# Kernel optimization log

Measured on AMD Instinct MI355X. Metric: run time of the kernel, lower is better.

## Reference

```python
import jax, jax.numpy as jnp
import numpy as np


def _make_coord(n):
    # pixel-center coords in [-1, 1] (LIIF-style make_coord)
    r = 1.0 / n
    return -1.0 + r + 2.0 * r * jnp.arange(n, dtype=jnp.float32)


def _grid_sample_bilinear(g, xs, ys):
    # g: (Cg, Gh, Gw); xs: (W,) x-coords in [-1,1]; ys: (H,) y-coords.
    # align_corners=True mapping: [-1,1] -> [0, size-1]
    Cg, Gh, Gw = g.shape
    ix = (xs + 1.0) * 0.5 * (Gw - 1)
    iy = (ys + 1.0) * 0.5 * (Gh - 1)
    ix0 = jnp.clip(jnp.floor(ix).astype(jnp.int32), 0, Gw - 1)
    iy0 = jnp.clip(jnp.floor(iy).astype(jnp.int32), 0, Gh - 1)
    ix1 = jnp.clip(ix0 + 1, 0, Gw - 1)
    iy1 = jnp.clip(iy0 + 1, 0, Gh - 1)
    wx = ix - ix0.astype(jnp.float32)  # (W,)
    wy = iy - iy0.astype(jnp.float32)  # (H,)
    # gather 4 corners -> (Cg, H, W)
    g00 = g[:, iy0[:, None], ix0[None, :]]
    g01 = g[:, iy0[:, None], ix1[None, :]]
    g10 = g[:, iy1[:, None], ix0[None, :]]
    g11 = g[:, iy1[:, None], ix1[None, :]]
    wx = wx[None, None, :]
    wy = wy[None, :, None]
    return (g00 * (1 - wy) * (1 - wx) + g01 * (1 - wy) * wx
            + g10 * wy * (1 - wx) + g11 * wy * wx)


def setup_inputs() -> dict:
    key = jax.random.key(0)
    ks = jax.random.split(key, 12)
    B, C, H, W = 8, 32, 256, 256
    hidden, out_dim = 64, 3
    tot_in = C + 16 * 4
    inp = {
        "feat": jax.random.normal(ks[0], (B, C, H, W), dtype=jnp.float32),
        "g0": jax.random.normal(ks[1], (16, 32, 32), dtype=jnp.float32) * 0.1,
        "g1": jax.random.normal(ks[2], (16, 64, 64), dtype=jnp.float32) * 0.1,
        "g2": jax.random.normal(ks[3], (16, 128, 128), dtype=jnp.float32) * 0.1,
        "g3": jax.random.normal(ks[4], (16, 256, 256), dtype=jnp.float32) * 0.1,
        "w1": jax.random.normal(ks[5], (hidden, tot_in), dtype=jnp.float32) * (1.0 / np.sqrt(tot_in)),
        "b1": jnp.zeros((hidden,), dtype=jnp.float32),
        "w2": jax.random.normal(ks[6], (hidden, hidden), dtype=jnp.float32) * (1.0 / np.sqrt(hidden)),
        "b2": jnp.zeros((hidden,), dtype=jnp.float32),
        "w3": jax.random.normal(ks[7], (out_dim, hidden), dtype=jnp.float32) * (1.0 / np.sqrt(hidden)),
        "b3": jnp.zeros((out_dim,), dtype=jnp.float32),
    }
    return inp


def reference(feat, g0, g1, g2, g3, w1, b1, w2, b2, w3, b3):
    B, C, H, W = feat.shape
    xs = _make_coord(W)
    ys = _make_coord(H)
    # grids are shared across batch (expand in torch) -> compute once
    local = jnp.concatenate(
        [_grid_sample_bilinear(g, xs, ys) for g in (g0, g1, g2, g3)], axis=0)  # (64,H,W)
    combined = jnp.concatenate(
        [feat, jnp.broadcast_to(local[None], (B,) + local.shape)], axis=1)  # (B,C+64,H,W)
    x = combined.transpose(0, 2, 3, 1)  # (B,H,W,C+64)
    h = jax.nn.relu(x @ w1.T + b1)
    h = jax.nn.relu(h @ w2.T + b2)
    out = h @ w3.T + b3
    return out.transpose(0, 3, 1, 2)  # (B,out_dim,H,W)
```

## Files before the change

### kernel.cpp

```cpp
#include <hip/hip_runtime.h>
#include <hip/hip_bf16.h>


typedef float f32x4 __attribute__((ext_vector_type(4)));
typedef short s16x8 __attribute__((ext_vector_type(8)));

#define MFMA16(a, b, c) __builtin_amdgcn_mfma_f32_16x16x32_bf16((a), (b), (c), 0, 0, 0)

__device__ __forceinline__ short bfbits(float f) {
    return __builtin_bit_cast(short, __float2bfloat16(f));
}

__device__ __forceinline__ s16x8 pack_relu(const f32x4 lo, const f32x4 hi) {
    s16x8 r;
#pragma unroll
    for (int e = 0; e < 4; ++e) {
        r[e]     = bfbits(fmaxf(lo[e], 0.0f));
        r[e + 4] = bfbits(fmaxf(hi[e], 0.0f));
    }
    return r;
}

#define NFRAG 22

__global__ __launch_bounds__(256, 4) void grid_inr_mfma(
    const float* __restrict__ feat,
    const float* __restrict__ g0, const float* __restrict__ g1,
    const float* __restrict__ g2, const float* __restrict__ g3,
    const float* __restrict__ w1, const float* __restrict__ b1,
    const float* __restrict__ w2, const float* __restrict__ b2,
    const float* __restrict__ w3, const float* __restrict__ b3,
    float* __restrict__ out)
{
    __shared__ __align__(16) short lds_w[NFRAG * 64 * 8];

    const int lane  = threadIdx.x & 63;
    const int col   = lane & 15;
    const int lrow  = lane >> 4;
    const int wv    = threadIdx.x >> 6;
    const int p     = blockIdx.x * 64 + wv * 16 + col;

    {
        const int cs = lane, c15 = lane & 15, r4 = lane >> 4;
#pragma unroll 1
        for (int fid = threadIdx.x >> 6; fid < NFRAG; fid += 4) {
            const float* src;
            if (fid < 12) {
                const int mt = fid / 3, kb = fid - 3 * mt;
                src = w1 + (16 * mt + c15) * 96 + 32 * kb + 4 * r4;
            } else if (fid < 20) {
                const int f = fid - 12, mt = f >> 1, kb = f & 1;
                src = w2 + (16 * mt + c15) * 64 + 32 * kb + 4 * r4;
            } else {
                const int kb = fid - 20;
                const int row3 = (c15 < 3) ? c15 : 2;
                src = w3 + row3 * 64 + 32 * kb + 4 * r4;
            }
            s16x8 frag;
#pragma unroll
            for (int e = 0; e < 8; ++e)
                frag[e] = bfbits(src[(e & 3) + 16 * (e >> 2)]);
            *(s16x8*)&lds_w[(fid * 64 + cs) * 8] = frag;
        }
    }

    f32x4 b1f[4], b2f[4];
#pragma unroll
    for (int mt = 0; mt < 4; ++mt) {
        b1f[mt] = *(const f32x4*)(b1 + 16 * mt + 4 * lrow);
        b2f[mt] = *(const f32x4*)(b2 + 16 * mt + 4 * lrow);
    }
    const float b3s0 = b3[0], b3s1 = b3[1], b3s2 = b3[2];

    s16x8 localB[2];
    {
        const float* gs[4] = {g0, g1, g2, g3};
        const int    gn[4] = {32, 64, 128, 256};
        const int px = p & 255;
        const int py = p >> 8;
#pragma unroll
        for (int lv = 0; lv < 4; ++lv) {
            const int G = gn[lv];
            const float ix = (float)((2 * px + 1) * (G - 1)) * (1.0f / 512.0f);
            const float iy = (float)((2 * py + 1) * (G - 1)) * (1.0f / 512.0f);
            int ix0 = (int)ix;
            int iy0 = (int)iy;
            if (ix0 > G - 1) ix0 = G - 1;
            if (iy0 > G - 1) iy0 = G - 1;
            const int ix1 = (ix0 + 1 < G - 1) ? (ix0 + 1) : (G - 1);
            const int iy1 = (iy0 + 1 < G - 1) ? (iy0 + 1) : (G - 1);
            const float wx = ix - (float)ix0;
            const float wy = iy - (float)iy0;
            const float w00 = (1.0f - wy) * (1.0f - wx);
            const float w01 = (1.0f - wy) * wx;
            const float w10 = wy * (1.0f - wx);
            const float w11 = wy * wx;
            const int o00 = iy0 * G + ix0;
            const int o01 = iy0 * G + ix1;
            const int o10 = iy1 * G + ix0;
            const int o11 = iy1 * G + ix1;
            const float* g = gs[lv];
            const int GG = G * G;
#pragma unroll
            for (int j = 0; j < 4; ++j) {
                const float* gc = g + (4 * lrow + j) * GG;
                const float v = gc[o00] * w00 + gc[o01] * w01 +
                                gc[o10] * w10 + gc[o11] * w11;
                localB[lv >> 1][(lv & 1) * 4 + j] = bfbits(v);
            }
        }
    }

    __syncthreads();

    const short* lw = lds_w + lane * 8;
#define LDSFRAG(fid) (*(const s16x8*)(lw + (fid) * 64 * 8))

    s16x8 w1ff[4], w3f[2];
#pragma unroll
    for (int mt = 0; mt < 4; ++mt) w1ff[mt] = LDSFRAG(mt * 3);
    w3f[0] = LDSFRAG(20);
    w3f[1] = LDSFRAG(21);

    f32x4 c1base[4];
#pragma unroll
    for (int mt = 0; mt < 4; ++mt) {
        c1base[mt] = b1f[mt];
        c1base[mt] = MFMA16(LDSFRAG(mt * 3 + 1), localB[0], c1base[mt]);
        c1base[mt] = MFMA16(LDSFRAG(mt * 3 + 2), localB[1], c1base[mt]);
    }

    auto process = [&](int b, const s16x8 ff) {
        f32x4 c1[4];
#pragma unroll
        for (int mt = 0; mt < 4; ++mt)
            c1[mt] = MFMA16(w1ff[mt], ff, c1base[mt]);

        s16x8 h1b0 = pack_relu(c1[0], c1[1]);
        s16x8 h1b1 = pack_relu(c1[2], c1[3]);

        f32x4 c2[4];
#pragma unroll
        for (int mt = 0; mt < 4; ++mt) {
            c2[mt] = b2f[mt];
            c2[mt] = MFMA16(LDSFRAG(12 + mt * 2),     h1b0, c2[mt]);
            c2[mt] = MFMA16(LDSFRAG(12 + mt * 2 + 1), h1b1, c2[mt]);
        }
        s16x8 h2b0 = pack_relu(c2[0], c2[1]);
        s16x8 h2b1 = pack_relu(c2[2], c2[3]);

        f32x4 c3 = {0.f, 0.f, 0.f, 0.f};
        c3 = MFMA16(w3f[0], h2b0, c3);
        c3 = MFMA16(w3f[1], h2b1, c3);

        if (lrow == 0) {
            out[((b * 3 + 0) << 16) + p] = c3[0] + b3s0;
            out[((b * 3 + 1) << 16) + p] = c3[1] + b3s1;
            out[((b * 3 + 2) << 16) + p] = c3[2] + b3s2;
        }
    };

    float rawP[8], rawQ[8];
#pragma unroll
    for (int e = 0; e < 8; ++e) {
        const int fc = 4 * lrow + (e & 3) + 16 * (e >> 2);
        rawP[e] = feat[(fc << 16) + p];
        rawQ[e] = feat[((32 + fc) << 16) + p];
    }

#pragma unroll 1
    for (int bp = 0; bp < 4; ++bp) {
        s16x8 ff;
#pragma unroll
        for (int e = 0; e < 8; ++e) ff[e] = bfbits(rawP[e]);
        if (bp < 3) {
#pragma unroll
            for (int e = 0; e < 8; ++e) {
                const int fc = 4 * lrow + (e & 3) + 16 * (e >> 2);
                rawP[e] = feat[((((2 * bp + 2) << 5) | fc) << 16) + p];
            }
        }
        process(2 * bp, ff);

#pragma unroll
        for (int e = 0; e < 8; ++e) ff[e] = bfbits(rawQ[e]);
        if (bp < 3) {
#pragma unroll
            for (int e = 0; e < 8; ++e) {
                const int fc = 4 * lrow + (e & 3) + 16 * (e >> 2);
                rawQ[e] = feat[((((2 * bp + 3) << 5) | fc) << 16) + p];
            }
        }
        process(2 * bp + 1, ff);
    }
#undef LDSFRAG
}

extern "C" void kernel_launch(void* const* d_in, const int* in_sizes, int n_in,
                              void* d_out, int out_size, void* d_ws, size_t ws_size,
                              hipStream_t stream) {
    const float* feat = (const float*)d_in[0];
    const float* g0   = (const float*)d_in[1];
    const float* g1   = (const float*)d_in[2];
    const float* g2   = (const float*)d_in[3];
    const float* g3   = (const float*)d_in[4];
    const float* w1   = (const float*)d_in[5];
    const float* b1   = (const float*)d_in[6];
    const float* w2   = (const float*)d_in[7];
    const float* b2   = (const float*)d_in[8];
    const float* w3   = (const float*)d_in[9];
    const float* b3   = (const float*)d_in[10];

    grid_inr_mfma<<<1024, 256, 0, stream>>>(
        feat, g0, g1, g2, g3, w1, b1, w2, b2, w3, b3, (float*)d_out);
}
```

Before: 28.75 us.

## Software-pipeline MLP layer-1 across batches and move b2 and weight frags to LDS

Restructures the batch loop so the layer-1 MFMAs for the next batch run while the current batch's layer-2/3 tail runs, interleaving independent MFMA chains. The b2 bias moves to LDS and the w1ff/w3 fragments are re-read from LDS instead of living in registers, which cuts register pressure at the cost of extra LDS reads. The initial feature loads are issued before the barrier so global latency overlaps the weight staging.

```diff
diff --git a/kernel.cpp b/kernel.cpp
--- a/kernel.cpp
+++ b/kernel.cpp
@@ -33,6 +33,7 @@
     float* __restrict__ out)
 {
     __shared__ __align__(16) short lds_w[NFRAG * 64 * 8];
+    __shared__ __align__(16) float lds_b2[64];
 
     const int lane  = threadIdx.x & 63;
     const int col   = lane & 15;
@@ -40,6 +41,7 @@
     const int wv    = threadIdx.x >> 6;
     const int p     = blockIdx.x * 64 + wv * 16 + col;
 
+    if (threadIdx.x < 64) lds_b2[threadIdx.x] = b2[threadIdx.x];
     {
         const int cs = lane, c15 = lane & 15, r4 = lane >> 4;
 #pragma unroll 1
@@ -64,12 +66,6 @@
         }
     }
 
-    f32x4 b1f[4], b2f[4];
-#pragma unroll
-    for (int mt = 0; mt < 4; ++mt) {
-        b1f[mt] = *(const f32x4*)(b1 + 16 * mt + 4 * lrow);
-        b2f[mt] = *(const f32x4*)(b2 + 16 * mt + 4 * lrow);
-    }
     const float b3s0 = b3[0], b3s1 = b3[1], b3s2 = b3[2];
 
     s16x8 localB[2];
@@ -111,48 +107,40 @@
         }
     }
 
+    float rawP[8], rawQ[8];
+#pragma unroll
+    for (int e = 0; e < 8; ++e) {
+        const int fc = 4 * lrow + (e & 3) + 16 * (e >> 2);
+        rawP[e] = feat[(fc << 16) + p];
+        rawQ[e] = feat[((32 + fc) << 16) + p];
+    }
+
     __syncthreads();
 
     const short* lw = lds_w + lane * 8;
 #define LDSFRAG(fid) (*(const s16x8*)(lw + (fid) * 64 * 8))
 
-    s16x8 w1ff[4], w3f[2];
-#pragma unroll
-    for (int mt = 0; mt < 4; ++mt) w1ff[mt] = LDSFRAG(mt * 3);
-    w3f[0] = LDSFRAG(20);
-    w3f[1] = LDSFRAG(21);
-
     f32x4 c1base[4];
 #pragma unroll
     for (int mt = 0; mt < 4; ++mt) {
-        c1base[mt] = b1f[mt];
+        c1base[mt] = *(const f32x4*)(b1 + 16 * mt + 4 * lrow);
         c1base[mt] = MFMA16(LDSFRAG(mt * 3 + 1), localB[0], c1base[mt]);
         c1base[mt] = MFMA16(LDSFRAG(mt * 3 + 2), localB[1], c1base[mt]);
     }
 
-    auto process = [&](int b, const s16x8 ff) {
-        f32x4 c1[4];
-#pragma unroll
-        for (int mt = 0; mt < 4; ++mt)
-            c1[mt] = MFMA16(w1ff[mt], ff, c1base[mt]);
-
-        s16x8 h1b0 = pack_relu(c1[0], c1[1]);
-        s16x8 h1b1 = pack_relu(c1[2], c1[3]);
-
+    auto tail = [&](int b, const s16x8 h0, const s16x8 h1) {
         f32x4 c2[4];
 #pragma unroll
         for (int mt = 0; mt < 4; ++mt) {
-            c2[mt] = b2f[mt];
-            c2[mt] = MFMA16(LDSFRAG(12 + mt * 2),     h1b0, c2[mt]);
-            c2[mt] = MFMA16(LDSFRAG(12 + mt * 2 + 1), h1b1, c2[mt]);
-        }
-        s16x8 h2b0 = pack_relu(c2[0], c2[1]);
-        s16x8 h2b1 = pack_relu(c2[2], c2[3]);
-
+            const f32x4 bb = *(const f32x4*)&lds_b2[16 * mt + 4 * lrow];
+            c2[mt] = MFMA16(LDSFRAG(12 + 2 * mt + 1), h1,
+                            MFMA16(LDSFRAG(12 + 2 * mt), h0, bb));
+        }
+        const s16x8 h2b0 = pack_relu(c2[0], c2[1]);
+        const s16x8 h2b1 = pack_relu(c2[2], c2[3]);
         f32x4 c3 = {0.f, 0.f, 0.f, 0.f};
-        c3 = MFMA16(w3f[0], h2b0, c3);
-        c3 = MFMA16(w3f[1], h2b1, c3);
-
+        c3 = MFMA16(LDSFRAG(20), h2b0, c3);
+        c3 = MFMA16(LDSFRAG(21), h2b1, c3);
         if (lrow == 0) {
             out[((b * 3 + 0) << 16) + p] = c3[0] + b3s0;
             out[((b * 3 + 1) << 16) + p] = c3[1] + b3s1;
@@ -160,38 +148,61 @@
         }
     };
 
-    float rawP[8], rawQ[8];
-#pragma unroll
-    for (int e = 0; e < 8; ++e) {
-        const int fc = 4 * lrow + (e & 3) + 16 * (e >> 2);
-        rawP[e] = feat[(fc << 16) + p];
-        rawQ[e] = feat[((32 + fc) << 16) + p];
+    f32x4 c1A[4], c1B[4];
+    {
+        s16x8 ffA;
+#pragma unroll
+        for (int e = 0; e < 8; ++e) ffA[e] = bfbits(rawP[e]);
+#pragma unroll
+        for (int e = 0; e < 8; ++e) {
+            const int fc = 4 * lrow + (e & 3) + 16 * (e >> 2);
+            rawP[e] = feat[(((2 << 5) | fc) << 16) + p];
+        }
+#pragma unroll
+        for (int mt = 0; mt < 4; ++mt)
+            c1A[mt] = MFMA16(LDSFRAG(mt * 3), ffA, c1base[mt]);
     }
 
 #pragma unroll 1
     for (int bp = 0; bp < 4; ++bp) {
-        s16x8 ff;
-#pragma unroll
-        for (int e = 0; e < 8; ++e) ff[e] = bfbits(rawP[e]);
-        if (bp < 3) {
-#pragma unroll
-            for (int e = 0; e < 8; ++e) {
-                const int fc = 4 * lrow + (e & 3) + 16 * (e >> 2);
-                rawP[e] = feat[((((2 * bp + 2) << 5) | fc) << 16) + p];
-            }
-        }
-        process(2 * bp, ff);
-
-#pragma unroll
-        for (int e = 0; e < 8; ++e) ff[e] = bfbits(rawQ[e]);
-        if (bp < 3) {
-#pragma unroll
-            for (int e = 0; e < 8; ++e) {
-                const int fc = 4 * lrow + (e & 3) + 16 * (e >> 2);
-                rawQ[e] = feat[((((2 * bp + 3) << 5) | fc) << 16) + p];
-            }
-        }
-        process(2 * bp + 1, ff);
+        {
+            const s16x8 h1A0 = pack_relu(c1A[0], c1A[1]);
+            const s16x8 h1A1 = pack_relu(c1A[2], c1A[3]);
+            s16x8 ffB;
+#pragma unroll
+            for (int e = 0; e < 8; ++e) ffB[e] = bfbits(rawQ[e]);
+            if (bp < 3) {
+#pragma unroll
+                for (int e = 0; e < 8; ++e) {
+                    const int fc = 4 * lrow + (e & 3) + 16 * (e >> 2);
+                    rawQ[e] = feat[((((2 * bp + 3) << 5) | fc) << 16) + p];
+                }
+            }
+#pragma unroll
+            for (int mt = 0; mt < 4; ++mt)
+                c1B[mt] = MFMA16(LDSFRAG(mt * 3), ffB, c1base[mt]);
+            tail(2 * bp, h1A0, h1A1);
+        }
+        {
+            const s16x8 h1B0 = pack_relu(c1B[0], c1B[1]);
+            const s16x8 h1B1 = pack_relu(c1B[2], c1B[3]);
+            if (bp < 3) {
+                s16x8 ffA;
+#pragma unroll
+                for (int e = 0; e < 8; ++e) ffA[e] = bfbits(rawP[e]);
+                if (bp < 2) {
+#pragma unroll
+                    for (int e = 0; e < 8; ++e) {
+                        const int fc = 4 * lrow + (e & 3) + 16 * (e >> 2);
+                        rawP[e] = feat[((((2 * bp + 4) << 5) | fc) << 16) + p];
+                    }
+                }
+#pragma unroll
+                for (int mt = 0; mt < 4; ++mt)
+                    c1A[mt] = MFMA16(LDSFRAG(mt * 3), ffA, c1base[mt]);
+            }
+            tail(2 * bp + 1, h1B0, h1B1);
+        }
     }
 #undef LDSFRAG
 }
```

Measured after the change: 51.06 us. 1.78x slower.

## Split batch across two grid rows and reduce register pressure for occupancy

Applied to the files above, without the earlier changes.

The batch of 8 is split into two halves along blockIdx.y, so each block handles 4 batches and the grid doubles to 2048 blocks. Prefetch drops from two register buffers to one, and the W1/W3 fragments are read from LDS on every use instead of being held in registers. Launch bounds go from 4 to 5 waves per SIMD. The aim is more parallelism and higher occupancy to hide feat load latency. The cost is that weight staging and the grid-sample interpolation are now repeated in twice as many blocks, and the loop issues more LDS reads.

```diff
diff --git a/kernel.cpp b/kernel.cpp
--- a/kernel.cpp
+++ b/kernel.cpp
@@ -23,7 +23,7 @@
 
 #define NFRAG 22
 
-__global__ __launch_bounds__(256, 4) void grid_inr_mfma(
+__global__ __launch_bounds__(256, 5) void grid_inr_mfma(
     const float* __restrict__ feat,
     const float* __restrict__ g0, const float* __restrict__ g1,
     const float* __restrict__ g2, const float* __restrict__ g3,
@@ -39,6 +39,7 @@
     const int lrow  = lane >> 4;
     const int wv    = threadIdx.x >> 6;
     const int p     = blockIdx.x * 64 + wv * 16 + col;
+    const int b0    = blockIdx.y * 4;
 
     {
         const int cs = lane, c15 = lane & 15, r4 = lane >> 4;
@@ -111,16 +112,17 @@
         }
     }
 
+    float raw[8];
+#pragma unroll
+    for (int e = 0; e < 8; ++e) {
+        const int fc = 4 * lrow + (e & 3) + 16 * (e >> 2);
+        raw[e] = feat[(((b0 << 5) | fc) << 16) + p];
+    }
+
     __syncthreads();
 
     const short* lw = lds_w + lane * 8;
 #define LDSFRAG(fid) (*(const s16x8*)(lw + (fid) * 64 * 8))
-
-    s16x8 w1ff[4], w3f[2];
-#pragma unroll
-    for (int mt = 0; mt < 4; ++mt) w1ff[mt] = LDSFRAG(mt * 3);
-    w3f[0] = LDSFRAG(20);
-    w3f[1] = LDSFRAG(21);
 
     f32x4 c1base[4];
 #pragma unroll
@@ -130,11 +132,25 @@
         c1base[mt] = MFMA16(LDSFRAG(mt * 3 + 2), localB[1], c1base[mt]);
     }
 
-    auto process = [&](int b, const s16x8 ff) {
+#pragma unroll 1
+    for (int bi = 0; bi < 4; ++bi) {
+        const int b = b0 + bi;
+
+        s16x8 ff;
+#pragma unroll
+        for (int e = 0; e < 8; ++e) ff[e] = bfbits(raw[e]);
+        if (bi < 3) {
+#pragma unroll
+            for (int e = 0; e < 8; ++e) {
+                const int fc = 4 * lrow + (e & 3) + 16 * (e >> 2);
+                raw[e] = feat[((((b + 1) << 5) | fc) << 16) + p];
+            }
+        }
+
         f32x4 c1[4];
 #pragma unroll
         for (int mt = 0; mt < 4; ++mt)
-            c1[mt] = MFMA16(w1ff[mt], ff, c1base[mt]);
+            c1[mt] = MFMA16(LDSFRAG(mt * 3), ff, c1base[mt]);
 
         s16x8 h1b0 = pack_relu(c1[0], c1[1]);
         s16x8 h1b1 = pack_relu(c1[2], c1[3]);
@@ -150,48 +166,14 @@
         s16x8 h2b1 = pack_relu(c2[2], c2[3]);
 
         f32x4 c3 = {0.f, 0.f, 0.f, 0.f};
-        c3 = MFMA16(w3f[0], h2b0, c3);
-        c3 = MFMA16(w3f[1], h2b1, c3);
+        c3 = MFMA16(LDSFRAG(20), h2b0, c3);
+        c3 = MFMA16(LDSFRAG(21), h2b1, c3);
 
         if (lrow == 0) {
             out[((b * 3 + 0) << 16) + p] = c3[0] + b3s0;
             out[((b * 3 + 1) << 16) + p] = c3[1] + b3s1;
             out[((b * 3 + 2) << 16) + p] = c3[2] + b3s2;
         }
-    };
-
-    float rawP[8], rawQ[8];
-#pragma unroll
-    for (int e = 0; e < 8; ++e) {
-        const int fc = 4 * lrow + (e & 3) + 16 * (e >> 2);
-        rawP[e] = feat[(fc << 16) + p];
-        rawQ[e] = feat[((32 + fc) << 16) + p];
-    }
-
-#pragma unroll 1
-    for (int bp = 0; bp < 4; ++bp) {
-        s16x8 ff;
-#pragma unroll
-        for (int e = 0; e < 8; ++e) ff[e] = bfbits(rawP[e]);
-        if (bp < 3) {
-#pragma unroll
-            for (int e = 0; e < 8; ++e) {
-                const int fc = 4 * lrow + (e & 3) + 16 * (e >> 2);
-                rawP[e] = feat[((((2 * bp + 2) << 5) | fc) << 16) + p];
-            }
-        }
-        process(2 * bp, ff);
-
-#pragma unroll
-        for (int e = 0; e < 8; ++e) ff[e] = bfbits(rawQ[e]);
-        if (bp < 3) {
-#pragma unroll
-            for (int e = 0; e < 8; ++e) {
-                const int fc = 4 * lrow + (e & 3) + 16 * (e >> 2);
-                rawQ[e] = feat[((((2 * bp + 3) << 5) | fc) << 16) + p];
-            }
-        }
-        process(2 * bp + 1, ff);
     }
 #undef LDSFRAG
 }
@@ -211,6 +193,7 @@
     const float* w3   = (const float*)d_in[9];
     const float* b3   = (const float*)d_in[10];
 
-    grid_inr_mfma<<<1024, 256, 0, stream>>>(
+    dim3 grid(1024, 2);
+    grid_inr_mfma<<<grid, 256, 0, stream>>>(
         feat, g0, g1, g2, g3, w1, b1, w2, b2, w3, b3, (float*)d_out);
 }
```

Result: slower. 75.65 us (+163.1%).

## Split into precompute kernel and batch-parallel MLP kernel via workspace

Applied to the files above, without the earlier changes.

Splits the fused kernel into two launches. The first computes the grid-sample features and their layer-1 partial products for each pixel, writes them to workspace, and has one block build a bf16 weight-fragment table. The second launches a 2D grid over pixels and batch pairs, reloads the weight table and partial sums, and runs the MLP for two batches per block. This is meant to expose more parallelism than the old serial loop over eight batches per thread. In exchange it writes and reads back a 16 MB partial-sum buffer and adds a second launch; the original fused kernel remains as a fallback when the workspace is too small.

```diff
diff --git a/kernel.cpp b/kernel.cpp
--- a/kernel.cpp
+++ b/kernel.cpp
@@ -21,38 +21,36 @@
     return r;
 }
 
-#define NFRAG 22
-
-__global__ __launch_bounds__(256, 4) void grid_inr_mfma(
-    const float* __restrict__ feat,
+#define WS_TAB_BYTES 16384
+#define NFRAG 14
+
+__global__ __launch_bounds__(256, 4) void k1_precomp(
     const float* __restrict__ g0, const float* __restrict__ g1,
     const float* __restrict__ g2, const float* __restrict__ g3,
     const float* __restrict__ w1, const float* __restrict__ b1,
-    const float* __restrict__ w2, const float* __restrict__ b2,
-    const float* __restrict__ w3, const float* __restrict__ b3,
-    float* __restrict__ out)
+    const float* __restrict__ w2, const float* __restrict__ w3,
+    void* __restrict__ ws)
 {
-    __shared__ __align__(16) short lds_w[NFRAG * 64 * 8];
-
     const int lane  = threadIdx.x & 63;
     const int col   = lane & 15;
     const int lrow  = lane >> 4;
     const int wv    = threadIdx.x >> 6;
     const int p     = blockIdx.x * 64 + wv * 16 + col;
 
-    {
-        const int cs = lane, c15 = lane & 15, r4 = lane >> 4;
+    if (blockIdx.x == 0) {
+        short* wtab = (short*)ws;
 #pragma unroll 1
-        for (int fid = threadIdx.x >> 6; fid < NFRAG; fid += 4) {
+        for (int i = threadIdx.x; i < NFRAG * 64; i += 256) {
+            const int fid = i >> 6, l = i & 63;
+            const int c15 = l & 15, r4 = l >> 4;
             const float* src;
-            if (fid < 12) {
-                const int mt = fid / 3, kb = fid - 3 * mt;
-                src = w1 + (16 * mt + c15) * 96 + 32 * kb + 4 * r4;
-            } else if (fid < 20) {
-                const int f = fid - 12, mt = f >> 1, kb = f & 1;
+            if (fid < 4) {
+                src = w1 + (16 * fid + c15) * 96 + 4 * r4;
+            } else if (fid < 12) {
+                const int f = fid - 4, mt = f >> 1, kb = f & 1;
                 src = w2 + (16 * mt + c15) * 64 + 32 * kb + 4 * r4;
             } else {
-                const int kb = fid - 20;
+                const int kb = fid - 12;
                 const int row3 = (c15 < 3) ? c15 : 2;
                 src = w3 + row3 * 64 + 32 * kb + 4 * r4;
             }
@@ -60,17 +58,9 @@
 #pragma unroll
             for (int e = 0; e < 8; ++e)
                 frag[e] = bfbits(src[(e & 3) + 16 * (e >> 2)]);
-            *(s16x8*)&lds_w[(fid * 64 + cs) * 8] = frag;
-        }
-    }
-
-    f32x4 b1f[4], b2f[4];
-#pragma unroll
-    for (int mt = 0; mt < 4; ++mt) {
-        b1f[mt] = *(const f32x4*)(b1 + 16 * mt + 4 * lrow);
-        b2f[mt] = *(const f32x4*)(b2 + 16 * mt + 4 * lrow);
-    }
-    const float b3s0 = b3[0], b3s1 = b3[1], b3s2 = b3[2];
+            *(s16x8*)&wtab[i * 8] = frag;
+        }
+    }
 
     s16x8 localB[2];
     {
@@ -111,17 +101,228 @@
         }
     }
 
+    f32x4 c1base[4];
+#pragma unroll
+    for (int mt = 0; mt < 4; ++mt) {
+        c1base[mt] = *(const f32x4*)(b1 + 16 * mt + 4 * lrow);
+#pragma unroll
+        for (int kb = 1; kb <= 2; ++kb) {
+            const float* wr = w1 + (16 * mt + col) * 96 + 32 * kb + 4 * lrow;
+            const f32x4 lo = *(const f32x4*)(wr);
+            const f32x4 hi = *(const f32x4*)(wr + 16);
+            s16x8 frag;
+#pragma unroll
+            for (int e = 0; e < 4; ++e) {
+                frag[e]     = bfbits(lo[e]);
+                frag[e + 4] = bfbits(hi[e]);
+            }
+            c1base[mt] = MFMA16(frag, localB[kb - 1], c1base[mt]);
+        }
+    }
+
+    f32x4* wsc = (f32x4*)((char*)ws + WS_TAB_BYTES);
+#pragma unroll
+    for (int mt = 0; mt < 4; ++mt)
+        wsc[(mt * 4 + lrow) * 65536 + p] = c1base[mt];
+}
+
+__global__ __launch_bounds__(256, 6) void k2_mlp(
+    const float* __restrict__ feat,
+    const float* __restrict__ b2, const float* __restrict__ b3,
+    const void* __restrict__ ws, float* __restrict__ out)
+{
+    __shared__ __align__(16) short lds_w[WS_TAB_BYTES / 2];
+
+    const int lane  = threadIdx.x & 63;
+    const int col   = lane & 15;
+    const int lrow  = lane >> 4;
+    const int wv    = threadIdx.x >> 6;
+    const int p     = blockIdx.x * 64 + wv * 16 + col;
+    const int bA    = blockIdx.y * 2;
+    const int bB    = bA + 1;
+
+    const f32x4* wtab = (const f32x4*)ws;
+    const f32x4 s0 = wtab[threadIdx.x];
+    const f32x4 s1 = wtab[threadIdx.x + 256];
+    const f32x4 s2 = wtab[threadIdx.x + 512];
+    const f32x4 s3 = wtab[threadIdx.x + 768];
+
+    const f32x4* wsc = (const f32x4*)((const char*)ws + WS_TAB_BYTES);
+    f32x4 c1base[4];
+#pragma unroll
+    for (int mt = 0; mt < 4; ++mt)
+        c1base[mt] = wsc[(mt * 4 + lrow) * 65536 + p];
+
+    float rawA[8], rawB[8];
+#pragma unroll
+    for (int e = 0; e < 8; ++e) {
+        const int fc = 4 * lrow + (e & 3) + 16 * (e >> 2);
+        rawA[e] = feat[(((bA << 5) | fc) << 16) + p];
+        rawB[e] = feat[(((bB << 5) | fc) << 16) + p];
+    }
+    const float b3s0 = b3[0], b3s1 = b3[1], b3s2 = b3[2];
+
+    f32x4* lw4 = (f32x4*)lds_w;
+    lw4[threadIdx.x]       = s0;
+    lw4[threadIdx.x + 256] = s1;
+    lw4[threadIdx.x + 512] = s2;
+    lw4[threadIdx.x + 768] = s3;
     __syncthreads();
 
+    const short* lwp = lds_w + lane * 8;
+#define LDSFRAG(fid) (*(const s16x8*)(lwp + (fid) * 64 * 8))
+
+    {
+        s16x8 ff;
+#pragma unroll
+        for (int e = 0; e < 8; ++e) ff[e] = bfbits(rawA[e]);
+        f32x4 c1[4];
+#pragma unroll
+        for (int mt = 0; mt < 4; ++mt)
+            c1[mt] = MFMA16(LDSFRAG(mt), ff, c1base[mt]);
+        const s16x8 h1b0 = pack_relu(c1[0], c1[1]);
+        const s16x8 h1b1 = pack_relu(c1[2], c1[3]);
+        f32x4 c2[4];
+#pragma unroll
+        for (int mt = 0; mt < 4; ++mt) {
+            c2[mt] = *(const f32x4*)(b2 + 16 * mt + 4 * lrow);
+            c2[mt] = MFMA16(LDSFRAG(4 + mt * 2),     h1b0, c2[mt]);
+            c2[mt] = MFMA16(LDSFRAG(4 + mt * 2 + 1), h1b1, c2[mt]);
+        }
+        const s16x8 h2b0 = pack_relu(c2[0], c2[1]);
+        const s16x8 h2b1 = pack_relu(c2[2], c2[3]);
+        f32x4 c3 = {0.f, 0.f, 0.f, 0.f};
+        c3 = MFMA16(LDSFRAG(12), h2b0, c3);
+        c3 = MFMA16(LDSFRAG(13), h2b1, c3);
+        if (lrow == 0) {
+            out[((bA * 3 + 0) << 16) + p] = c3[0] + b3s0;
+            out[((bA * 3 + 1) << 16) + p] = c3[1] + b3s1;
+            out[((bA * 3 + 2) << 16) + p] = c3[2] + b3s2;
+        }
+    }
+    {
+        s16x8 ff;
+#pragma unroll
+        for (int e = 0; e < 8; ++e) ff[e] = bfbits(rawB[e]);
+        f32x4 c1[4];
+#pragma unroll
+        for (int mt = 0; mt < 4; ++mt)
+            c1[mt] = MFMA16(LDSFRAG(mt), ff, c1base[mt]);
+        const s16x8 h1b0 = pack_relu(c1[0], c1[1]);
+        const s16x8 h1b1 = pack_relu(c1[2], c1[3]);
+        f32x4 c2[4];
+#pragma unroll
+        for (int mt = 0; mt < 4; ++mt) {
+            c2[mt] = *(const f32x4*)(b2 + 16 * mt + 4 * lrow);
+            c2[mt] = MFMA16(LDSFRAG(4 + mt * 2),     h1b0, c2[mt]);
+            c2[mt] = MFMA16(LDSFRAG(4 + mt * 2 + 1), h1b1, c2[mt]);
+        }
+        const s16x8 h2b0 = pack_relu(c2[0], c2[1]);
+        const s16x8 h2b1 = pack_relu(c2[2], c2[3]);
+        f32x4 c3 = {0.f, 0.f, 0.f, 0.f};
+        c3 = MFMA16(LDSFRAG(12), h2b0, c3);
+        c3 = MFMA16(LDSFRAG(13), h2b1, c3);
+        if (lrow == 0) {
+            out[((bB * 3 + 0) << 16) + p] = c3[0] + b3s0;
+            out[((bB * 3 + 1) << 16) + p] = c3[1] + b3s1;
+            out[((bB * 3 + 2) << 16) + p] = c3[2] + b3s2;
+        }
+    }
+#undef LDSFRAG
+}
+
+#define R6NFRAG 22
+__global__ __launch_bounds__(256, 4) void grid_inr_r6(
+    const float* __restrict__ feat,
+    const float* __restrict__ g0, const float* __restrict__ g1,
+    const float* __restrict__ g2, const float* __restrict__ g3,
+    const float* __restrict__ w1, const float* __restrict__ b1,
+    const float* __restrict__ w2, const float* __restrict__ b2,
+    const float* __restrict__ w3, const float* __restrict__ b3,
+    float* __restrict__ out)
+{
+    __shared__ __align__(16) short lds_w[R6NFRAG * 64 * 8];
+    const int lane  = threadIdx.x & 63;
+    const int col   = lane & 15;
+    const int lrow  = lane >> 4;
+    const int wv    = threadIdx.x >> 6;
+    const int p     = blockIdx.x * 64 + wv * 16 + col;
+    {
+        const int cs = lane, c15 = lane & 15, r4 = lane >> 4;
+#pragma unroll 1
+        for (int fid = threadIdx.x >> 6; fid < R6NFRAG; fid += 4) {
+            const float* src;
+            if (fid < 12) {
+                const int mt = fid / 3, kb = fid - 3 * mt;
+                src = w1 + (16 * mt + c15) * 96 + 32 * kb + 4 * r4;
+            } else if (fid < 20) {
+                const int f = fid - 12, mt = f >> 1, kb = f & 1;
+                src = w2 + (16 * mt + c15) * 64 + 32 * kb + 4 * r4;
+            } else {
+                const int kb = fid - 20;
+                const int row3 = (c15 < 3) ? c15 : 2;
+                src = w3 + row3 * 64 + 32 * kb + 4 * r4;
+            }
+            s16x8 frag;
+#pragma unroll
+            for (int e = 0; e < 8; ++e)
+                frag[e] = bfbits(src[(e & 3) + 16 * (e >> 2)]);
+            *(s16x8*)&lds_w[(fid * 64 + cs) * 8] = frag;
+        }
+    }
+    f32x4 b1f[4], b2f[4];
+#pragma unroll
+    for (int mt = 0; mt < 4; ++mt) {
+        b1f[mt] = *(const f32x4*)(b1 + 16 * mt + 4 * lrow);
+        b2f[mt] = *(const f32x4*)(b2 + 16 * mt + 4 * lrow);
+    }
+    const float b3s0 = b3[0], b3s1 = b3[1], b3s2 = b3[2];
+    s16x8 localB[2];
+    {
+        const float* gs[4] = {g0, g1, g2, g3};
+        const int    gn[4] = {32, 64, 128, 256};
+        const int px = p & 255;
+        const int py = p >> 8;
+#pragma unroll
+        for (int lv = 0; lv < 4; ++lv) {
+            const int G = gn[lv];
+            const float ix = (float)((2 * px + 1) * (G - 1)) * (1.0f / 512.0f);
+            const float iy = (float)((2 * py + 1) * (G - 1)) * (1.0f / 512.0f);
+            int ix0 = (int)ix;
+            int iy0 = (int)iy;
+            if (ix0 > G - 1) ix0 = G - 1;
+            if (iy0 > G - 1) iy0 = G - 1;
+            const int ix1 = (ix0 + 1 < G - 1) ? (ix0 + 1) : (G - 1);
+            const int iy1 = (iy0 + 1 < G - 1) ? (iy0 + 1) : (G - 1);
+            const float wx = ix - (float)ix0;
+            const float wy = iy - (float)iy0;
+            const float w00 = (1.0f - wy) * (1.0f - wx);
+            const float w01 = (1.0f - wy) * wx;
+            const float w10 = wy * (1.0f - wx);
+            const float w11 = wy * wx;
+            const int o00 = iy0 * G + ix0;
+            const int o01 = iy0 * G + ix1;
+            const int o10 = iy1 * G + ix0;
+            const int o11 = iy1 * G + ix1;
+            const float* g = gs[lv];
+            const int GG = G * G;
+#pragma unroll
+            for (int j = 0; j < 4; ++j) {
+                const float* gc = g + (4 * lrow + j) * GG;
+                const float v = gc[o00] * w00 + gc[o01] * w01 +
+                                gc[o10] * w10 + gc[o11] * w11;
+                localB[lv >> 1][(lv & 1) * 4 + j] = bfbits(v);
+            }
+        }
+    }
+    __syncthreads();
     const short* lw = lds_w + lane * 8;
 #define LDSFRAG(fid) (*(const s16x8*)(lw + (fid) * 64 * 8))
-
     s16x8 w1ff[4], w3f[2];
 #pragma unroll
     for (int mt = 0; mt < 4; ++mt) w1ff[mt] = LDSFRAG(mt * 3);
     w3f[0] = LDSFRAG(20);
     w3f[1] = LDSFRAG(21);
-
     f32x4 c1base[4];
 #pragma unroll
     for (int mt = 0; mt < 4; ++mt) {
@@ -129,16 +330,13 @@
         c1base[mt] = MFMA16(LDSFRAG(mt * 3 + 1), localB[0], c1base[mt]);
         c1base[mt] = MFMA16(LDSFRAG(mt * 3 + 2), localB[1], c1base[mt]);
     }
-
     auto process = [&](int b, const s16x8 ff) {
         f32x4 c1[4];
 #pragma unroll
         for (int mt = 0; mt < 4; ++mt)
             c1[mt] = MFMA16(w1ff[mt], ff, c1base[mt]);
-
         s16x8 h1b0 = pack_relu(c1[0], c1[1]);
         s16x8 h1b1 = pack_relu(c1[2], c1[3]);
-
         f32x4 c2[4];
 #pragma unroll
         for (int mt = 0; mt < 4; ++mt) {
@@ -148,18 +346,15 @@
         }
         s16x8 h2b0 = pack_relu(c2[0], c2[1]);
         s16x8 h2b1 = pack_relu(c2[2], c2[3]);
-
         f32x4 c3 = {0.f, 0.f, 0.f, 0.f};
         c3 = MFMA16(w3f[0], h2b0, c3);
         c3 = MFMA16(w3f[1], h2b1, c3);
-
         if (lrow == 0) {
             out[((b * 3 + 0) << 16) + p] = c3[0] + b3s0;
             out[((b * 3 + 1) << 16) + p] = c3[1] + b3s1;
             out[((b * 3 + 2) << 16) + p] = c3[2] + b3s2;
         }
     };
-
     float rawP[8], rawQ[8];
 #pragma unroll
     for (int e = 0; e < 8; ++e) {
@@ -167,7 +362,6 @@
         rawP[e] = feat[(fc << 16) + p];
         rawQ[e] = feat[((32 + fc) << 16) + p];
     }
-
 #pragma unroll 1
     for (int bp = 0; bp < 4; ++bp) {
         s16x8 ff;
@@ -181,7 +375,6 @@
             }
         }
         process(2 * bp, ff);
-
 #pragma unroll
         for (int e = 0; e < 8; ++e) ff[e] = bfbits(rawQ[e]);
         if (bp < 3) {
@@ -211,6 +404,13 @@
     const float* w3   = (const float*)d_in[9];
     const float* b3   = (const float*)d_in[10];
 
-    grid_inr_mfma<<<1024, 256, 0, stream>>>(
-        feat, g0, g1, g2, g3, w1, b1, w2, b2, w3, b3, (float*)d_out);
-}
+    const size_t need = (size_t)WS_TAB_BYTES + (size_t)16 * 65536 * 16;
+    if (ws_size >= need) {
+        k1_precomp<<<1024, 256, 0, stream>>>(g0, g1, g2, g3, w1, b1, w2, w3, d_ws);
+        dim3 g2grid(1024, 4);
+        k2_mlp<<<g2grid, 256, 0, stream>>>(feat, b2, b3, d_ws, (float*)d_out);
+    } else {
+        grid_inr_r6<<<1024, 256, 0, stream>>>(
+            feat, g0, g1, g2, g3, w1, b1, w2, b2, w3, b3, (float*)d_out);
+    }
+}
```

Result: slower. 59.70 us (+107.6%).
